# Kernel tuning notes

Hardware: AMD Instinct MI355X
Metric: run time of the kernel (lower is better)

Reference implementation:

```python
import jax, jax.numpy as jnp
import numpy as np

D_MODEL = 4096
N_HEAD = 32
N_KV_HEAD = 8
D_HEAD = D_MODEL // N_HEAD  # 128
B, T = 2, 2048


def setup_inputs() -> dict:
    key = jax.random.key(0)
    ks = jax.random.split(key, 6)
    x = jax.random.normal(ks[0], (B, T, D_MODEL), dtype=jnp.float32)
    # RoPE angles: theta_i = 10000^(-2i/d_head), angle = pos * theta_i
    inv_freq = 1.0 / (10000.0 ** (jnp.arange(0, D_HEAD, 2, dtype=jnp.float32) / D_HEAD))
    angles = jnp.arange(T, dtype=jnp.float32)[:, None] * inv_freq[None, :]  # [T, D_HEAD//2]
    freqs_cos = jnp.cos(angles)
    freqs_sin = jnp.sin(angles)
    s = 0.02
    wq = jax.random.normal(ks[1], (D_MODEL, N_HEAD * D_HEAD), dtype=jnp.float32) * s
    wk = jax.random.normal(ks[2], (D_MODEL, N_KV_HEAD * D_HEAD), dtype=jnp.float32) * s
    wv = jax.random.normal(ks[3], (D_MODEL, N_KV_HEAD * D_HEAD), dtype=jnp.float32) * s
    wo = jax.random.normal(ks[4], (D_MODEL, D_MODEL), dtype=jnp.float32) * s
    return {"x": x, "freqs_cos": freqs_cos, "freqs_sin": freqs_sin,
            "wq": wq, "wk": wk, "wv": wv, "wo": wo}


def _apply_rope(xq, xk, cos, sin):
    # xq: [B,T,Hq,D], xk: [B,T,Hk,D]; cos/sin: [T, D//2]
    def rot(t):
        tr = t.astype(jnp.float32).reshape(*t.shape[:-1], -1, 2)  # [B,T,H,D//2,2]
        xr, xi = tr[..., 0], tr[..., 1]
        c = cos[None, :, None, :]
        s = sin[None, :, None, :]
        out_r = xr * c - xi * s
        out_i = xr * s + xi * c
        return jnp.stack([out_r, out_i], axis=-1).reshape(t.shape).astype(t.dtype)
    return rot(xq), rot(xk)


def reference(x, freqs_cos, freqs_sin, wq, wk, wv, wo):
    Bq, Tq, _ = x.shape
    xq = (x @ wq).reshape(Bq, Tq, N_HEAD, D_HEAD)
    xk = (x @ wk).reshape(Bq, Tq, N_KV_HEAD, D_HEAD)
    xv = (x @ wv).reshape(Bq, Tq, N_KV_HEAD, D_HEAD)
    xq, xk = _apply_rope(xq, xk, freqs_cos, freqs_sin)
    # [B,H,T,D]
    xq = xq.transpose(0, 2, 1, 3)
    xk = xk.transpose(0, 2, 1, 3)
    xv = xv.transpose(0, 2, 1, 3)
    # GQA: repeat kv heads
    rep = N_HEAD // N_KV_HEAD
    xk = jnp.repeat(xk, rep, axis=1)
    xv = jnp.repeat(xv, rep, axis=1)
    scale = 1.0 / np.sqrt(D_HEAD)
    scores = jnp.einsum("bhqd,bhkd->bhqk", xq, xk) * scale
    causal = jnp.tril(jnp.ones((Tq, Tq), dtype=bool))
    scores = jnp.where(causal[None, None], scores, jnp.finfo(scores.dtype).min)
    probs = jax.nn.softmax(scores, axis=-1)
    z = jnp.einsum("bhqk,bhkd->bhqd", probs, xv)
    z = z.transpose(0, 2, 1, 3).reshape(Bq, Tq, D_MODEL)
    return z @ wo
```

## Files before the change

### kernel.cpp

```cpp
#include <hip/hip_runtime.h>

typedef unsigned short u16;
typedef unsigned int u32;
typedef u16 u16x8 __attribute__((ext_vector_type(8)));
typedef __bf16 bf16x8 __attribute__((ext_vector_type(8)));
typedef float f32x4 __attribute__((ext_vector_type(4)));

#define TOKENS 4096
#define DMODEL 4096
#define QKVN 6144
#define NHEAD 32
#define NKV 8
#define DHEAD 128
#define SEQ 2048

__device__ inline u16 f2bf(float f) {
    unsigned int u = __float_as_uint(f);
    u += 0x7fffu + ((u >> 16) & 1u);
    return (u16)(u >> 16);
}
__device__ inline float bf2f(u16 h) {
    return __uint_as_float(((unsigned int)h) << 16);
}
__device__ inline u32 pack2bf(float a, float b) {
    return (u32)f2bf(a) | ((u32)f2bf(b) << 16);
}
__device__ inline f32x4 mfma16(bf16x8 a, bf16x8 b, f32x4 c) {
    return __builtin_amdgcn_mfma_f32_16x16x32_bf16(a, b, c, 0, 0, 0);
}
__device__ __forceinline__ void gload16(const u16* g, u16* l) {
    __builtin_amdgcn_global_load_lds((const __attribute__((address_space(1))) u32*)g,
                                     (__attribute__((address_space(3))) u32*)l, 16, 0, 0);
}

__global__ __launch_bounds__(256) void f2bf_kernel(const float* __restrict__ in,
                                                   u16* __restrict__ out, int n) {
    int i = (blockIdx.x * 256 + threadIdx.x) * 4;
    if (i >= n) return;
    float4 v = *(const float4*)(in + i);
    u16 o0 = f2bf(v.x), o1 = f2bf(v.y), o2 = f2bf(v.z), o3 = f2bf(v.w);
    u16* p = out + i;
    p[0] = o0; p[1] = o1; p[2] = o2; p[3] = o3;
}

__global__ __launch_bounds__(256) void transpose_kernel(const float* __restrict__ in,
                                                        u16* __restrict__ out,
                                                        int K, int N) {
    __shared__ float t[32][33];
    int n0 = blockIdx.x * 32, k0 = blockIdx.y * 32;
    int x = threadIdx.x, y = threadIdx.y;
#pragma unroll
    for (int i = 0; i < 4; i++)
        t[y + 8 * i][x] = in[(size_t)(k0 + y + 8 * i) * N + n0 + x];
    __syncthreads();
#pragma unroll
    for (int i = 0; i < 4; i++)
        out[(size_t)(n0 + y + 8 * i) * K + k0 + x] = f2bf(t[x][y + 8 * i]);
}

__global__ __launch_bounds__(256) void vtrans_kernel(const u16* __restrict__ qkv,
                                                     u16* __restrict__ vt) {
    __shared__ u16 t[32][33];
    int b = blockIdx.z;
    int c0 = blockIdx.x * 32;
    int r0 = blockIdx.y * 32;
    int x = threadIdx.x, y = threadIdx.y;
    const u16* in = qkv + (size_t)(b * SEQ) * QKVN + 5120;
#pragma unroll
    for (int i = 0; i < 4; i++)
        t[y + 8 * i][x] = in[(size_t)(r0 + y + 8 * i) * QKVN + c0 + x];
    __syncthreads();
    u16* out = vt + (size_t)b * 1024 * SEQ;
#pragma unroll
    for (int i = 0; i < 4; i++)
        out[(size_t)(c0 + y + 8 * i) * SEQ + r0 + x] = t[x][y + 8 * i];
}

template <bool OUT_F32>
__global__ __launch_bounds__(256, 2) void gemm_lds(const u16* __restrict__ A,
                                                   const u16* __restrict__ Bt,
                                                   void* __restrict__ C,
                                                   int M, int N, int K) {
    __shared__ u16 lA[128 * 32];
    __shared__ u16 lB[128 * 32];
    int tid = threadIdx.x, wave = tid >> 6, lane = tid & 63;
    int quad = lane >> 4, l16 = lane & 15;
    int m0 = blockIdx.y * 128, n0 = blockIdx.x * 128;
    int wm = (wave >> 1) * 64, wn = (wave & 1) * 64;
    int lrow = lane >> 2, lcol = (lane & 3) * 8;

    const u16* ga = A + (size_t)(m0 + wave * 32 + lrow) * K + lcol;
    const u16* gb = Bt + (size_t)(n0 + wave * 32 + lrow) * K + lcol;
    u16* la = lA + (wave * 32) * 32;
    u16* lb = lB + (wave * 32) * 32;

    f32x4 acc[4][4] = {};

    gload16(ga, la);
    gload16(ga + (size_t)16 * K, la + 512);
    gload16(gb, lb);
    gload16(gb + (size_t)16 * K, lb + 512);

    for (int k0 = 0; k0 < K; k0 += 32) {
        __syncthreads();
        bf16x8 af[4], bfr[4];
#pragma unroll
        for (int i = 0; i < 4; i++)
            af[i] = *(const bf16x8*)(lA + (wm + i * 16 + l16) * 32 + quad * 8);
#pragma unroll
        for (int j = 0; j < 4; j++)
            bfr[j] = *(const bf16x8*)(lB + (wn + j * 16 + l16) * 32 + quad * 8);
        if (k0 + 32 < K) {
            __syncthreads();
            gload16(ga + k0 + 32, la);
            gload16(ga + (size_t)16 * K + k0 + 32, la + 512);
            gload16(gb + k0 + 32, lb);
            gload16(gb + (size_t)16 * K + k0 + 32, lb + 512);
        }
#pragma unroll
        for (int i = 0; i < 4; i++)
#pragma unroll
            for (int j = 0; j < 4; j++)
                acc[i][j] = mfma16(af[i], bfr[j], acc[i][j]);
    }

#pragma unroll
    for (int i = 0; i < 4; i++)
#pragma unroll
        for (int j = 0; j < 4; j++) {
            int row = m0 + wm + i * 16 + quad * 4;
            int col = n0 + wn + j * 16 + l16;
            if (OUT_F32) {
                float* Cf = (float*)C;
#pragma unroll
                for (int r = 0; r < 4; r++)
                    Cf[(size_t)(row + r) * N + col] = acc[i][j][r];
            } else {
                u16* Cb = (u16*)C;
#pragma unroll
                for (int r = 0; r < 4; r++)
                    Cb[(size_t)(row + r) * N + col] = f2bf(acc[i][j][r]);
            }
        }
}

__global__ __launch_bounds__(256) void rope2_kernel(u16* __restrict__ buf,
                                                    const float* __restrict__ cosb,
                                                    const float* __restrict__ sinb,
                                                    int nheads, int colbase, float scale) {
    int idx = blockIdx.x * 256 + threadIdx.x;
    int p = idx & 63;
    int rest = idx >> 6;
    int h = rest & (nheads - 1);
    int tok = rest / nheads;
    int tseq = tok & (SEQ - 1);
    float c = cosb[tseq * 64 + p], s = sinb[tseq * 64 + p];
    u32* ptr = (u32*)(buf + (size_t)tok * QKVN + colbase + h * DHEAD + 2 * p);
    u32 v = *ptr;
    float xr = bf2f((u16)(v & 0xffff)), xi = bf2f((u16)(v >> 16));
    float orr = (xr * c - xi * s) * scale;
    float oii = (xr * s + xi * c) * scale;
    *ptr = pack2bf(orr, oii);
}

#define LDP 72
#define NINF (-__builtin_inff())

__global__ __launch_bounds__(256, 2) void flash2_kernel(const u16* __restrict__ QKV,
                                                        const u16* __restrict__ Vt,
                                                        u16* __restrict__ Z) {
    __shared__ u16 lK[4][64 * 32];
    __shared__ u16 lV[2][128 * 32];
    __shared__ u16 lP[4][32 * LDP];
    int tid = threadIdx.x, wave = tid >> 6, lane = tid & 63;
    int quad = lane >> 4, l16 = lane & 15;
    int qt = 15 - (int)blockIdx.x;
    int h = blockIdx.y, b = blockIdx.z;
    int kvh = h >> 2;
    int Q0 = qt * 128;
    int qw = Q0 + wave * 32;
    int lrow = lane >> 2, lcol = (lane & 3) * 8;

    bf16x8 qf[2][4];
#pragma unroll
    for (int nt = 0; nt < 2; nt++) {
        const u16* qp = QKV + (size_t)(b * SEQ + qw + nt * 16 + l16) * QKVN + h * DHEAD;
#pragma unroll
        for (int kk = 0; kk < 4; kk++)
            qf[nt][kk] = *(const bf16x8*)(qp + kk * 32 + quad * 8);
    }

    f32x4 o[2][8] = {};
    float mrun[2] = {NINF, NINF};
    float lrun[2] = {0.f, 0.f};

    const u16* gk = QKV + (size_t)(b * SEQ + lrow) * QKVN + DMODEL + kvh * DHEAD + wave * 32 + lcol;
    u16* lk = lK[wave];
    int kf_w = wave >> 1, dh_w = (wave & 1) * 64;
    const u16* gv = Vt + ((size_t)(b * NKV + kvh) * DHEAD + dh_w + lrow) * SEQ + kf_w * 32 + lcol;
    u16* lv = lV[kf_w] + dh_w * 32;

    int nkt = 2 * qt + 2;
    for (int kt = 0; kt < nkt; kt++) {
        int key0 = kt * 64;
        if (kt) __syncthreads();
#pragma unroll
        for (int g = 0; g < 4; g++)
            gload16(gk + (size_t)(key0 + g * 16) * QKVN, lk + g * 512);
#pragma unroll
        for (int g = 0; g < 4; g++)
            gload16(gv + (size_t)(g * 16) * SEQ + key0, lv + g * 512);
        __syncthreads();

        if (key0 <= qw + 31) {
            f32x4 st[4][2] = {};
#pragma unroll
            for (int kk = 0; kk < 4; kk++) {
                bf16x8 kfr[4];
#pragma unroll
                for (int mt = 0; mt < 4; mt++)
                    kfr[mt] = *(const bf16x8*)(lK[kk] + (mt * 16 + l16) * 32 + quad * 8);
#pragma unroll
                for (int mt = 0; mt < 4; mt++)
#pragma unroll
                    for (int nt = 0; nt < 2; nt++)
                        st[mt][nt] = mfma16(kfr[mt], qf[nt][kk], st[mt][nt]);
            }
            if (key0 + 63 > qw) {
#pragma unroll
                for (int mt = 0; mt < 4; mt++)
#pragma unroll
                    for (int nt = 0; nt < 2; nt++)
#pragma unroll
                        for (int r = 0; r < 4; r++)
                            if (key0 + mt * 16 + quad * 4 + r > qw + nt * 16 + l16)
                                st[mt][nt][r] = NINF;
            }
            float alpha[2];
#pragma unroll
            for (int nt = 0; nt < 2; nt++) {
                float vmax = NINF;
#pragma unroll
                for (int mt = 0; mt < 4; mt++)
#pragma unroll
                    for (int r = 0; r < 4; r++) vmax = fmaxf(vmax, st[mt][nt][r]);
                vmax = fmaxf(vmax, __shfl_xor(vmax, 16));
                vmax = fmaxf(vmax, __shfl_xor(vmax, 32));
                float mnew = fmaxf(mrun[nt], vmax);
                alpha[nt] = __expf(mrun[nt] - mnew);
                mrun[nt] = mnew;
                float rsum = 0.f;
#pragma unroll
                for (int mt = 0; mt < 4; mt++)
#pragma unroll
                    for (int r = 0; r < 4; r++) {
                        float p = __expf(st[mt][nt][r] - mnew);
                        st[mt][nt][r] = p;
                        rsum += p;
                    }
                rsum += __shfl_xor(rsum, 16);
                rsum += __shfl_xor(rsum, 32);
                lrun[nt] = lrun[nt] * alpha[nt] + rsum;
#pragma unroll
                for (int mt = 0; mt < 4; mt++) {
                    u32 p01 = pack2bf(st[mt][nt][0], st[mt][nt][1]);
                    u32 p23 = pack2bf(st[mt][nt][2], st[mt][nt][3]);
                    uint2 pk; pk.x = p01; pk.y = p23;
                    *(uint2*)(lP[wave] + (nt * 16 + l16) * LDP + mt * 16 + quad * 4) = pk;
                }
            }
#pragma unroll
            for (int mtq = 0; mtq < 2; mtq++)
#pragma unroll
                for (int r = 0; r < 4; r++) {
                    float av = __shfl(alpha[mtq], quad * 4 + r);
#pragma unroll
                    for (int ntd = 0; ntd < 8; ntd++) o[mtq][ntd][r] *= av;
                }
#pragma unroll
            for (int kfi = 0; kfi < 2; kfi++) {
                bf16x8 pf0 = *(const bf16x8*)(lP[wave] + l16 * LDP + kfi * 32 + quad * 8);
                bf16x8 pf1 = *(const bf16x8*)(lP[wave] + (16 + l16) * LDP + kfi * 32 + quad * 8);
#pragma unroll
                for (int ntd = 0; ntd < 8; ntd++) {
                    bf16x8 vfr = *(const bf16x8*)(lV[kfi] + (ntd * 16 + l16) * 32 + quad * 8);
                    o[0][ntd] = mfma16(pf0, vfr, o[0][ntd]);
                    o[1][ntd] = mfma16(pf1, vfr, o[1][ntd]);
                }
            }
        }
    }
#pragma unroll
    for (int mtq = 0; mtq < 2; mtq++) {
        float linv[4];
#pragma unroll
        for (int r = 0; r < 4; r++) linv[r] = 1.0f / __shfl(lrun[mtq], quad * 4 + r);
#pragma unroll
        for (int ntd = 0; ntd < 8; ntd++)
#pragma unroll
            for (int r = 0; r < 4; r++) {
                int q = qw + mtq * 16 + quad * 4 + r;
                Z[(size_t)(b * SEQ + q) * DMODEL + h * DHEAD + ntd * 16 + l16] =
                    f2bf(o[mtq][ntd][r] * linv[r]);
            }
    }
}

extern "C" void kernel_launch(void* const* d_in, const int* in_sizes, int n_in,
                              void* d_out, int out_size, void* d_ws, size_t ws_size,
                              hipStream_t stream) {
    const float* x    = (const float*)d_in[0];
    const float* fcos = (const float*)d_in[1];
    const float* fsin = (const float*)d_in[2];
    const float* wq   = (const float*)d_in[3];
    const float* wk   = (const float*)d_in[4];
    const float* wv   = (const float*)d_in[5];
    const float* wo   = (const float*)d_in[6];
    float* out = (float*)d_out;
    char* ws = (char*)d_ws;

    const size_t MiB = 1024ull * 1024ull;
    u16* xb    = (u16*)(ws);
    u16* zb    = xb;
    u16* wqkvt = (u16*)(ws + 32 * MiB);
    u16* wot   = (u16*)(ws + 80 * MiB);
    u16* qkv   = (u16*)(ws + 112 * MiB);
    u16* vtb   = (u16*)(ws + 160 * MiB);

    f2bf_kernel<<<16384, 256, 0, stream>>>(x, xb, TOKENS * DMODEL);
    dim3 tb(32, 8);
    transpose_kernel<<<dim3(128, 128), tb, 0, stream>>>(wq, wqkvt, 4096, 4096);
    transpose_kernel<<<dim3(32, 128), tb, 0, stream>>>(wk, wqkvt + (size_t)4096 * 4096, 4096, 1024);
    transpose_kernel<<<dim3(32, 128), tb, 0, stream>>>(wv, wqkvt + (size_t)5120 * 4096, 4096, 1024);
    transpose_kernel<<<dim3(128, 128), tb, 0, stream>>>(wo, wot, 4096, 4096);

    gemm_lds<false><<<dim3(48, 32), 256, 0, stream>>>(xb, wqkvt, qkv, 4096, QKVN, 4096);

    rope2_kernel<<<32768, 256, 0, stream>>>(qkv, fcos, fsin, NHEAD, 0, 0.08838834764831845f);
    rope2_kernel<<<8192, 256, 0, stream>>>(qkv, fcos, fsin, NKV, DMODEL, 1.0f);

    vtrans_kernel<<<dim3(32, 64, 2), tb, 0, stream>>>(qkv, vtb);

    flash2_kernel<<<dim3(16, 32, 2), 256, 0, stream>>>(qkv, vtb, zb);

    gemm_lds<true><<<dim3(32, 32), 256, 0, stream>>>(zb, wot, out, 4096, 4096, 4096);
}
```

Baseline: 843.4 us.

## Swizzle GEMM tiles, merge QKV weight transposes, restructure flash attention epilogue and softmax

Merges the three Q/K/V weight transpose launches into one kernel. Remaps GEMM block indices into grouped tiles so neighbouring blocks share A and B panels in cache. In attention it folds log2(e) into the Q scale and uses exp2, skips masking on fully visible 16x16 sub-tiles, and swaps the PV MFMA operands so alpha and row sums need no shuffles. It also stages the output through LDS for 16-byte coalesced Z stores. The main risks are the extra LDS round trip in the epilogue and the tile remap assuming grid dimensions divisible by 8 and 16.

```diff
diff --git a/kernel.cpp b/kernel.cpp
--- a/kernel.cpp
+++ b/kernel.cpp
@@ -22,7 +22,7 @@
 __device__ inline float bf2f(u16 h) {
     return __uint_as_float(((unsigned int)h) << 16);
 }
-__device__ inline u32 pack2bf(float a, float b) {
+__device__ inline u32 pk_bf2(float a, float b) {
     return (u32)f2bf(a) | ((u32)f2bf(b) << 16);
 }
 __device__ inline f32x4 mfma16(bf16x8 a, bf16x8 b, f32x4 c) {
@@ -56,6 +56,26 @@
 #pragma unroll
     for (int i = 0; i < 4; i++)
         out[(size_t)(n0 + y + 8 * i) * K + k0 + x] = f2bf(t[x][y + 8 * i]);
+}
+
+__global__ __launch_bounds__(256) void wqkv_trans_kernel(const float* __restrict__ wq,
+                                                         const float* __restrict__ wk,
+                                                         const float* __restrict__ wv,
+                                                         u16* __restrict__ out) {
+    __shared__ float t[32][33];
+    int n0 = blockIdx.x * 32, k0 = blockIdx.y * 32;
+    const float* src; int srcN, nc;
+    if (n0 < 4096)      { src = wq; srcN = 4096; nc = n0; }
+    else if (n0 < 5120) { src = wk; srcN = 1024; nc = n0 - 4096; }
+    else                { src = wv; srcN = 1024; nc = n0 - 5120; }
+    int x = threadIdx.x, y = threadIdx.y;
+#pragma unroll
+    for (int i = 0; i < 4; i++)
+        t[y + 8 * i][x] = src[(size_t)(k0 + y + 8 * i) * srcN + nc + x];
+    __syncthreads();
+#pragma unroll
+    for (int i = 0; i < 4; i++)
+        out[(size_t)(n0 + y + 8 * i) * 4096 + k0 + x] = f2bf(t[x][y + 8 * i]);
 }
 
 __global__ __launch_bounds__(256) void vtrans_kernel(const u16* __restrict__ qkv,
@@ -85,21 +105,26 @@
     __shared__ u16 lB[128 * 32];
     int tid = threadIdx.x, wave = tid >> 6, lane = tid & 63;
     int quad = lane >> 4, l16 = lane & 15;
-    int m0 = blockIdx.y * 128, n0 = blockIdx.x * 128;
+    int lb = blockIdx.y * gridDim.x + blockIdx.x;
+    int scols = gridDim.x >> 3;
+    int s = lb >> 7, r = lb & 127;
+    int bn = (s % scols) * 8 + (r & 7);
+    int bm = (s / scols) * 16 + (r >> 3);
+    int m0 = bm * 128, n0 = bn * 128;
     int wm = (wave >> 1) * 64, wn = (wave & 1) * 64;
     int lrow = lane >> 2, lcol = (lane & 3) * 8;
 
     const u16* ga = A + (size_t)(m0 + wave * 32 + lrow) * K + lcol;
     const u16* gb = Bt + (size_t)(n0 + wave * 32 + lrow) * K + lcol;
     u16* la = lA + (wave * 32) * 32;
-    u16* lb = lB + (wave * 32) * 32;
+    u16* lb2 = lB + (wave * 32) * 32;
 
     f32x4 acc[4][4] = {};
 
     gload16(ga, la);
     gload16(ga + (size_t)16 * K, la + 512);
-    gload16(gb, lb);
-    gload16(gb + (size_t)16 * K, lb + 512);
+    gload16(gb, lb2);
+    gload16(gb + (size_t)16 * K, lb2 + 512);
 
     for (int k0 = 0; k0 < K; k0 += 32) {
         __syncthreads();
@@ -114,8 +139,8 @@
             __syncthreads();
             gload16(ga + k0 + 32, la);
             gload16(ga + (size_t)16 * K + k0 + 32, la + 512);
-            gload16(gb + k0 + 32, lb);
-            gload16(gb + (size_t)16 * K + k0 + 32, lb + 512);
+            gload16(gb + k0 + 32, lb2);
+            gload16(gb + (size_t)16 * K + k0 + 32, lb2 + 512);
         }
 #pragma unroll
         for (int i = 0; i < 4; i++)
@@ -133,13 +158,13 @@
             if (OUT_F32) {
                 float* Cf = (float*)C;
 #pragma unroll
-                for (int r = 0; r < 4; r++)
-                    Cf[(size_t)(row + r) * N + col] = acc[i][j][r];
+                for (int r2 = 0; r2 < 4; r2++)
+                    Cf[(size_t)(row + r2) * N + col] = acc[i][j][r2];
             } else {
                 u16* Cb = (u16*)C;
 #pragma unroll
-                for (int r = 0; r < 4; r++)
-                    Cb[(size_t)(row + r) * N + col] = f2bf(acc[i][j][r]);
+                for (int r2 = 0; r2 < 4; r2++)
+                    Cb[(size_t)(row + r2) * N + col] = f2bf(acc[i][j][r2]);
             }
         }
 }
@@ -158,20 +183,19 @@
     u32* ptr = (u32*)(buf + (size_t)tok * QKVN + colbase + h * DHEAD + 2 * p);
     u32 v = *ptr;
     float xr = bf2f((u16)(v & 0xffff)), xi = bf2f((u16)(v >> 16));
-    float orr = (xr * c - xi * s) * scale;
-    float oii = (xr * s + xi * c) * scale;
-    *ptr = pack2bf(orr, oii);
+    *ptr = pk_bf2((xr * c - xi * s) * scale, (xr * s + xi * c) * scale);
 }
 
 #define LDP 72
 #define NINF (-__builtin_inff())
 
-__global__ __launch_bounds__(256, 2) void flash2_kernel(const u16* __restrict__ QKV,
+__global__ __launch_bounds__(256, 2) void flash3_kernel(const u16* __restrict__ QKV,
                                                         const u16* __restrict__ Vt,
                                                         u16* __restrict__ Z) {
-    __shared__ u16 lK[4][64 * 32];
-    __shared__ u16 lV[2][128 * 32];
-    __shared__ u16 lP[4][32 * LDP];
+    __shared__ u16 sm[25600];
+    u16* lKb = sm;
+    u16* lVb = sm + 8192;
+    u16* lPb = sm + 16384;
     int tid = threadIdx.x, wave = tid >> 6, lane = tid & 63;
     int quad = lane >> 4, l16 = lane & 15;
     int qt = 15 - (int)blockIdx.x;
@@ -190,15 +214,16 @@
             qf[nt][kk] = *(const bf16x8*)(qp + kk * 32 + quad * 8);
     }
 
-    f32x4 o[2][8] = {};
+    f32x4 o[8][2] = {};
     float mrun[2] = {NINF, NINF};
     float lrun[2] = {0.f, 0.f};
 
     const u16* gk = QKV + (size_t)(b * SEQ + lrow) * QKVN + DMODEL + kvh * DHEAD + wave * 32 + lcol;
-    u16* lk = lK[wave];
+    u16* lk = lKb + wave * 2048;
     int kf_w = wave >> 1, dh_w = (wave & 1) * 64;
     const u16* gv = Vt + ((size_t)(b * NKV + kvh) * DHEAD + dh_w + lrow) * SEQ + kf_w * 32 + lcol;
-    u16* lv = lV[kf_w] + dh_w * 32;
+    u16* lv = lVb + kf_w * 4096 + dh_w * 32;
+    u16* lp = lPb + wave * (32 * LDP);
 
     int nkt = 2 * qt + 2;
     for (int kt = 0; kt < nkt; kt++) {
@@ -212,97 +237,107 @@
             gload16(gv + (size_t)(g * 16) * SEQ + key0, lv + g * 512);
         __syncthreads();
 
-        if (key0 <= qw + 31) {
-            f32x4 st[4][2] = {};
-#pragma unroll
-            for (int kk = 0; kk < 4; kk++) {
-                bf16x8 kfr[4];
-#pragma unroll
-                for (int mt = 0; mt < 4; mt++)
-                    kfr[mt] = *(const bf16x8*)(lK[kk] + (mt * 16 + l16) * 32 + quad * 8);
-#pragma unroll
-                for (int mt = 0; mt < 4; mt++)
-#pragma unroll
-                    for (int nt = 0; nt < 2; nt++)
-                        st[mt][nt] = mfma16(kfr[mt], qf[nt][kk], st[mt][nt]);
-            }
-            if (key0 + 63 > qw) {
-#pragma unroll
-                for (int mt = 0; mt < 4; mt++)
-#pragma unroll
-                    for (int nt = 0; nt < 2; nt++)
-#pragma unroll
-                        for (int r = 0; r < 4; r++)
-                            if (key0 + mt * 16 + quad * 4 + r > qw + nt * 16 + l16)
-                                st[mt][nt][r] = NINF;
-            }
-            float alpha[2];
+        if (key0 > qw + 31) continue;
+
+        f32x4 st[4][2] = {};
+#pragma unroll
+        for (int kk = 0; kk < 4; kk++) {
+            bf16x8 kfr[4];
+#pragma unroll
+            for (int mt = 0; mt < 4; mt++)
+                kfr[mt] = *(const bf16x8*)(lKb + kk * 2048 + (mt * 16 + l16) * 32 + quad * 8);
+#pragma unroll
+            for (int mt = 0; mt < 4; mt++)
+#pragma unroll
+                for (int nt = 0; nt < 2; nt++)
+                    st[mt][nt] = mfma16(kfr[mt], qf[nt][kk], st[mt][nt]);
+        }
+#pragma unroll
+        for (int mt = 0; mt < 4; mt++)
 #pragma unroll
             for (int nt = 0; nt < 2; nt++) {
-                float vmax = NINF;
-#pragma unroll
-                for (int mt = 0; mt < 4; mt++)
-#pragma unroll
-                    for (int r = 0; r < 4; r++) vmax = fmaxf(vmax, st[mt][nt][r]);
-                vmax = fmaxf(vmax, __shfl_xor(vmax, 16));
-                vmax = fmaxf(vmax, __shfl_xor(vmax, 32));
-                float mnew = fmaxf(mrun[nt], vmax);
-                alpha[nt] = __expf(mrun[nt] - mnew);
-                mrun[nt] = mnew;
-                float rsum = 0.f;
-#pragma unroll
-                for (int mt = 0; mt < 4; mt++)
-#pragma unroll
-                    for (int r = 0; r < 4; r++) {
-                        float p = __expf(st[mt][nt][r] - mnew);
-                        st[mt][nt][r] = p;
-                        rsum += p;
-                    }
-                rsum += __shfl_xor(rsum, 16);
-                rsum += __shfl_xor(rsum, 32);
-                lrun[nt] = lrun[nt] * alpha[nt] + rsum;
-#pragma unroll
-                for (int mt = 0; mt < 4; mt++) {
-                    u32 p01 = pack2bf(st[mt][nt][0], st[mt][nt][1]);
-                    u32 p23 = pack2bf(st[mt][nt][2], st[mt][nt][3]);
-                    uint2 pk; pk.x = p01; pk.y = p23;
-                    *(uint2*)(lP[wave] + (nt * 16 + l16) * LDP + mt * 16 + quad * 4) = pk;
+                int kmin = key0 + mt * 16, qmin = qw + nt * 16;
+                if (kmin + 15 <= qmin) continue;
+                if (kmin > qmin + 15) {
+                    st[mt][nt] = (f32x4){NINF, NINF, NINF, NINF};
+                } else {
+#pragma unroll
+                    for (int r = 0; r < 4; r++)
+                        if (kmin + quad * 4 + r > qmin + l16) st[mt][nt][r] = NINF;
                 }
             }
-#pragma unroll
-            for (int mtq = 0; mtq < 2; mtq++)
+        float alpha[2];
+#pragma unroll
+        for (int nt = 0; nt < 2; nt++) {
+            float vmax = NINF;
+#pragma unroll
+            for (int mt = 0; mt < 4; mt++)
+#pragma unroll
+                for (int r = 0; r < 4; r++) vmax = fmaxf(vmax, st[mt][nt][r]);
+            vmax = fmaxf(vmax, __shfl_xor(vmax, 16));
+            vmax = fmaxf(vmax, __shfl_xor(vmax, 32));
+            float mnew = fmaxf(mrun[nt], vmax);
+            alpha[nt] = __builtin_amdgcn_exp2f(mrun[nt] - mnew);
+            mrun[nt] = mnew;
+            float rsum = 0.f;
+#pragma unroll
+            for (int mt = 0; mt < 4; mt++)
 #pragma unroll
                 for (int r = 0; r < 4; r++) {
-                    float av = __shfl(alpha[mtq], quad * 4 + r);
-#pragma unroll
-                    for (int ntd = 0; ntd < 8; ntd++) o[mtq][ntd][r] *= av;
+                    float p = __builtin_amdgcn_exp2f(st[mt][nt][r] - mnew);
+                    st[mt][nt][r] = p;
+                    rsum += p;
                 }
-#pragma unroll
-            for (int kfi = 0; kfi < 2; kfi++) {
-                bf16x8 pf0 = *(const bf16x8*)(lP[wave] + l16 * LDP + kfi * 32 + quad * 8);
-                bf16x8 pf1 = *(const bf16x8*)(lP[wave] + (16 + l16) * LDP + kfi * 32 + quad * 8);
-#pragma unroll
-                for (int ntd = 0; ntd < 8; ntd++) {
-                    bf16x8 vfr = *(const bf16x8*)(lV[kfi] + (ntd * 16 + l16) * 32 + quad * 8);
-                    o[0][ntd] = mfma16(pf0, vfr, o[0][ntd]);
-                    o[1][ntd] = mfma16(pf1, vfr, o[1][ntd]);
-                }
+            rsum += __shfl_xor(rsum, 16);
+            rsum += __shfl_xor(rsum, 32);
+            lrun[nt] = lrun[nt] * alpha[nt] + rsum;
+#pragma unroll
+            for (int mt = 0; mt < 4; mt++) {
+                uint2 pk;
+                pk.x = pk_bf2(st[mt][nt][0], st[mt][nt][1]);
+                pk.y = pk_bf2(st[mt][nt][2], st[mt][nt][3]);
+                *(uint2*)(lp + (nt * 16 + l16) * LDP + mt * 16 + quad * 4) = pk;
             }
         }
+#pragma unroll
+        for (int dt = 0; dt < 8; dt++)
+#pragma unroll
+            for (int nt = 0; nt < 2; nt++)
+#pragma unroll
+                for (int r = 0; r < 4; r++) o[dt][nt][r] *= alpha[nt];
+#pragma unroll
+        for (int kfi = 0; kfi < 2; kfi++) {
+            bf16x8 pf0 = *(const bf16x8*)(lp + l16 * LDP + kfi * 32 + quad * 8);
+            bf16x8 pf1 = *(const bf16x8*)(lp + (16 + l16) * LDP + kfi * 32 + quad * 8);
+#pragma unroll
+            for (int dt = 0; dt < 8; dt++) {
+                bf16x8 vfr = *(const bf16x8*)(lVb + kfi * 4096 + (dt * 16 + l16) * 32 + quad * 8);
+                o[dt][0] = mfma16(vfr, pf0, o[dt][0]);
+                o[dt][1] = mfma16(vfr, pf1, o[dt][1]);
+            }
+        }
     }
-#pragma unroll
-    for (int mtq = 0; mtq < 2; mtq++) {
-        float linv[4];
-#pragma unroll
-        for (int r = 0; r < 4; r++) linv[r] = 1.0f / __shfl(lrun[mtq], quad * 4 + r);
-#pragma unroll
-        for (int ntd = 0; ntd < 8; ntd++)
-#pragma unroll
-            for (int r = 0; r < 4; r++) {
-                int q = qw + mtq * 16 + quad * 4 + r;
-                Z[(size_t)(b * SEQ + q) * DMODEL + h * DHEAD + ntd * 16 + l16] =
-                    f2bf(o[mtq][ntd][r] * linv[r]);
-            }
+
+    __syncthreads();
+    u16* ebuf = sm + wave * 4352;
+    float linv[2];
+    linv[0] = 1.0f / lrun[0];
+    linv[1] = 1.0f / lrun[1];
+#pragma unroll
+    for (int dt = 0; dt < 8; dt++)
+#pragma unroll
+        for (int nt = 0; nt < 2; nt++) {
+            uint2 pk;
+            pk.x = pk_bf2(o[dt][nt][0] * linv[nt], o[dt][nt][1] * linv[nt]);
+            pk.y = pk_bf2(o[dt][nt][2] * linv[nt], o[dt][nt][3] * linv[nt]);
+            *(uint2*)(ebuf + (nt * 16 + l16) * 136 + dt * 16 + quad * 4) = pk;
+        }
+    int eq = lane >> 1, ed = (lane & 1) * 8;
+    u16* zrow = Z + (size_t)(b * SEQ + qw + eq) * DMODEL + h * DHEAD + ed;
+#pragma unroll
+    for (int half = 0; half < 8; half++) {
+        u16x8 v = *(const u16x8*)(ebuf + eq * 136 + half * 16 + ed);
+        *(u16x8*)(zrow + half * 16) = v;
     }
 }
 
@@ -329,19 +364,17 @@
 
     f2bf_kernel<<<16384, 256, 0, stream>>>(x, xb, TOKENS * DMODEL);
     dim3 tb(32, 8);
-    transpose_kernel<<<dim3(128, 128), tb, 0, stream>>>(wq, wqkvt, 4096, 4096);
-    transpose_kernel<<<dim3(32, 128), tb, 0, stream>>>(wk, wqkvt + (size_t)4096 * 4096, 4096, 1024);
-    transpose_kernel<<<dim3(32, 128), tb, 0, stream>>>(wv, wqkvt + (size_t)5120 * 4096, 4096, 1024);
+    wqkv_trans_kernel<<<dim3(192, 128), tb, 0, stream>>>(wq, wk, wv, wqkvt);
     transpose_kernel<<<dim3(128, 128), tb, 0, stream>>>(wo, wot, 4096, 4096);
 
     gemm_lds<false><<<dim3(48, 32), 256, 0, stream>>>(xb, wqkvt, qkv, 4096, QKVN, 4096);
 
-    rope2_kernel<<<32768, 256, 0, stream>>>(qkv, fcos, fsin, NHEAD, 0, 0.08838834764831845f);
+    rope2_kernel<<<32768, 256, 0, stream>>>(qkv, fcos, fsin, NHEAD, 0, 0.12751744416163924f);
     rope2_kernel<<<8192, 256, 0, stream>>>(qkv, fcos, fsin, NKV, DMODEL, 1.0f);
 
     vtrans_kernel<<<dim3(32, 64, 2), tb, 0, stream>>>(qkv, vtb);
 
-    flash2_kernel<<<dim3(16, 32, 2), 256, 0, stream>>>(qkv, vtb, zb);
+    flash3_kernel<<<dim3(16, 32, 2), 256, 0, stream>>>(qkv, vtb, zb);
 
     gemm_lds<true><<<dim3(32, 32), 256, 0, stream>>>(zb, wot, out, 4096, 4096, 4096);
 }
```

New measurement: 889.9 us. +5.5%, slower.
